# Performance work log

Measured on AMD Instinct MI355X. Metric: run time of the kernel, lower is better.

The kernel has to match this reference:

```python
import jax, jax.numpy as jnp
import numpy as np

T = 16384
INPUT_SIZE = 1024
STATE_SIZE = 512

def _xavier(key, shape):
    fan_in, fan_out = shape[-1], shape[-2] if len(shape) > 1 else shape[-1]
    bound = float(np.sqrt(6.0 / (fan_in + fan_out)))
    return jax.random.uniform(key, shape, jnp.float32, -bound, bound)

def setup_inputs() -> dict:
    key = jax.random.key(0)
    ks = jax.random.split(key, 6)
    x = jax.random.normal(ks[0], (T, INPUT_SIZE), jnp.float32)
    weight_input = _xavier(ks[1], (STATE_SIZE, 4, INPUT_SIZE))
    weight_recur = _xavier(ks[2], (4, STATE_SIZE))
    bias = _xavier(ks[3], (4, STATE_SIZE))
    W_reg = _xavier(ks[4], (1, STATE_SIZE))
    b_reg = jnp.zeros((1,), jnp.float32)
    return {"x": x, "weight_input": weight_input, "weight_recur": weight_recur,
            "bias": bias, "W_reg": W_reg, "b_reg": b_reg}

def reference(x, weight_input, weight_recur, bias, W_reg, b_reg):
    S = weight_recur.shape[1]
    # Precompute per-step input contributions: u[t, g, s] = weight_input[s, g, :] . x[t]
    u = jnp.einsum('sgi,ti->tgs', weight_input, x)  # (T, 4, S)

    def step(carry, u_t):
        h, c = carry  # each (S,)
        # torch: addmm(bias, weight_recur, diag(h)) == bias + weight_recur * h
        gates = bias + weight_recur * h[None, :] + u_t  # (4, S)
        f, i, o, g = gates
        f = jax.nn.sigmoid(f)
        i = jax.nn.sigmoid(i)
        o = jax.nn.sigmoid(o)
        g = jnp.tanh(g)
        c1 = f * c + i * g           # torch: f @ diag(c) + i*g
        h1 = o * jnp.tanh(c1)        # torch: diag of o * tanh(diag(c1))
        return (h1, c1), (h1, c1)

    h0 = jnp.zeros((S,), x.dtype)
    c0 = jnp.zeros((S,), x.dtype)
    (_, _), (hs, cs) = jax.lax.scan(step, (h0, c0), u)
    h_n = jnp.concatenate([h0[None, :], hs], axis=0)  # (T+1, S)
    c_n = jnp.concatenate([c0[None, :], cs], axis=0)  # (T+1, S)
    q = h_n @ W_reg.T + b_reg  # (T+1, 1); dropout p=0 -> identity
    q_t = q[1:]                # (T, 1)
    return (q_t, h_n, c_n)
```

## Files before the change

### kernel.cpp

```cpp
#include <hip/hip_runtime.h>

typedef unsigned short u16;
typedef unsigned int u32;
typedef __attribute__((ext_vector_type(4))) unsigned short u16x4;
typedef __attribute__((ext_vector_type(8))) short short8;
typedef __attribute__((ext_vector_type(8))) __bf16 bf16x8;
typedef __attribute__((ext_vector_type(4))) float f32x4;

#define T_STEPS 16384
#define INP 1024
#define SDIM 512
#define NGEMM 2048
#define L2E 1.4426950408889634f

__device__ __forceinline__ u16 f2bf(float f) {
    unsigned u = __float_as_uint(f);
    return (u16)((u + 0x7fffu + ((u >> 16) & 1u)) >> 16);
}
__device__ __forceinline__ float bfhi(u32 d) { return __uint_as_float(d & 0xffff0000u); }
__device__ __forceinline__ float bflo(u32 d) { return __uint_as_float(d << 16); }

__device__ __forceinline__ void gload_lds16(const void* g, void* l) {
    __builtin_amdgcn_global_load_lds((const __attribute__((address_space(1))) unsigned*)g,
                                     (__attribute__((address_space(3))) unsigned*)l, 16, 0, 0);
}

__global__ void cvt_x(const float* __restrict__ x, u16* __restrict__ xb, long n4) {
    long i = (long)blockIdx.x * blockDim.x + threadIdx.x;
    long stride = (long)gridDim.x * blockDim.x;
    for (; i < n4; i += stride) {
        float4 v = ((const float4*)x)[i];
        u16x4 o;
        o.x = f2bf(v.x); o.y = f2bf(v.y); o.z = f2bf(v.z); o.w = f2bf(v.w);
        ((u16x4*)xb)[i] = o;
    }
}

__global__ void pack_w(const float* __restrict__ w, u16* __restrict__ wb) {
    int id = blockIdx.x * blockDim.x + threadIdx.x;
    int kv = id & 255;
    int n  = id >> 8;
    int g = n >> 9, s = n & 511;
    const float4 v = *(const float4*)(w + ((long)(s * 4 + g)) * INP + kv * 4);
    u16x4 o;
    o.x = f2bf(v.x); o.y = f2bf(v.y); o.z = f2bf(v.z); o.w = f2bf(v.w);
    *(u16x4*)(wb + (long)n * INP + kv * 4) = o;
}

__global__ __launch_bounds__(512, 2) void gemm_bt(const u16* __restrict__ A,
                                                  const u16* __restrict__ B,
                                                  const float* __restrict__ wrec,
                                                  const float* __restrict__ bsv,
                                                  u32* __restrict__ coef,
                                                  int M, int N, int K) {
    __shared__ u16 sA[5][256 * 32];
    __shared__ u16 sB[5][256 * 32];
    const int tid = threadIdx.x;
    const int nbx = N >> 8;
    const int nwg = gridDim.x;
    const int cpx = nwg >> 3;
    const int bid = ((int)blockIdx.x & 7) * cpx + ((int)blockIdx.x >> 3);
    const int bx = bid % nbx, by = bid / nbx;
    const long brow = (long)by << 8, bcol = (long)bx << 8;
    const int w = tid >> 6, lane = tid & 63;
    const int wr = w >> 2, wc = w & 3;
    const int r16 = lane & 15, kq = lane >> 4;

    const int row0  = w * 32 + (lane >> 2);
    const int sslot = lane & 3;
    const int chs   = sslot ^ ((row0 >> 1) & 3);
    const u16* gA0 = A + (brow + row0) * (long)K + chs * 8;
    const u16* gA1 = gA0 + 16 * (long)K;
    const u16* gB0 = B + (bcol + row0) * (long)K + chs * 8;
    const u16* gB1 = gB0 + 16 * (long)K;
    const int dst0 = row0 * 32 + sslot * 8;
    const int dst1 = dst0 + 16 * 32;

    const int slotR = kq ^ ((r16 >> 1) & 3);
    int aoff[8], boff[4];
    #pragma unroll
    for (int m = 0; m < 8; ++m)
        aoff[m] = (wr * 128 + m * 16 + r16) * 32 + slotR * 8;
    #pragma unroll
    for (int n = 0; n < 4; ++n)
        boff[n] = (wc * 64 + n * 16 + r16) * 32 + slotR * 8;

    f32x4 acc[8][4] = {};
    bf16x8 afr[8], bfr[4];

#define STAGE(BUF, koff) do { \
        gload_lds16(gA0 + (koff), &sA[BUF][dst0]); \
        gload_lds16(gA1 + (koff), &sA[BUF][dst1]); \
        gload_lds16(gB0 + (koff), &sB[BUF][dst0]); \
        gload_lds16(gB1 + (koff), &sB[BUF][dst1]); \
    } while (0)

#define ITER(BNXT, SBUF, SKOFF, WAITSTR, DOSTAGE, DOREAD) do { \
        __builtin_amdgcn_s_setprio(1); \
        _Pragma("unroll") for (int m_ = 0; m_ < 8; ++m_) { \
            _Pragma("unroll") for (int n_ = 0; n_ < 4; ++n_) \
                acc[m_][n_] = __builtin_amdgcn_mfma_f32_16x16x32_bf16(afr[m_], bfr[n_], acc[m_][n_], 0, 0, 0); \
            if (DOREAD) afr[m_] = *(const bf16x8*)&sA[BNXT][aoff[m_]]; \
        } \
        __builtin_amdgcn_s_setprio(0); \
        if (DOREAD) { \
            _Pragma("unroll") for (int n_ = 0; n_ < 4; ++n_) \
                bfr[n_] = *(const bf16x8*)&sB[BNXT][boff[n_]]; \
        } \
        asm volatile(WAITSTR ::: "memory"); \
        if (DOSTAGE) { STAGE(SBUF, SKOFF); } \
        __builtin_amdgcn_s_barrier(); \
    } while (0)

    STAGE(0, 0);
    STAGE(1, 32);
    STAGE(2, 64);
    STAGE(3, 96);
    asm volatile("s_waitcnt vmcnt(8)" ::: "memory");
    __builtin_amdgcn_s_barrier();
    afr[0] = *(const bf16x8*)&sA[0][aoff[0]];
    #pragma unroll
    for (int n_ = 0; n_ < 4; ++n_) bfr[n_] = *(const bf16x8*)&sB[0][boff[n_]];
    #pragma unroll
    for (int m_ = 1; m_ < 8; ++m_) afr[m_] = *(const bf16x8*)&sA[0][aoff[m_]];

    #pragma unroll 1
    for (int t = 0; t < 25; t += 5) {
        ITER(1, 4, (t + 4) * 32, "s_waitcnt vmcnt(4)", 1, 1);
        ITER(2, 0, (t + 5) * 32, "s_waitcnt vmcnt(4)", 1, 1);
        ITER(3, 1, (t + 6) * 32, "s_waitcnt vmcnt(4)", 1, 1);
        ITER(4, 2, (t + 7) * 32, "s_waitcnt vmcnt(4)", 1, 1);
        ITER(0, 3, (t + 8) * 32, "s_waitcnt vmcnt(4)", 1, 1);
    }
    ITER(1, 4, 29 * 32, "s_waitcnt vmcnt(4)", 1, 1);
    ITER(2, 0, 30 * 32, "s_waitcnt vmcnt(4)", 1, 1);
    ITER(3, 1, 31 * 32, "s_waitcnt vmcnt(4)", 1, 1);
    ITER(4, 0, 0,       "s_waitcnt vmcnt(4)", 0, 1);
    ITER(0, 0, 0,       "s_waitcnt vmcnt(0)", 0, 1);
    ITER(1, 0, 0,       "s_waitcnt vmcnt(0)", 0, 1);
    {
        __builtin_amdgcn_s_setprio(1);
        #pragma unroll
        for (int m_ = 0; m_ < 8; ++m_)
            #pragma unroll
            for (int n_ = 0; n_ < 4; ++n_)
                acc[m_][n_] = __builtin_amdgcn_mfma_f32_16x16x32_bf16(afr[m_], bfr[n_], acc[m_][n_], 0, 0, 0);
        __builtin_amdgcn_s_setprio(0);
    }
#undef ITER
#undef STAGE

    const int g = (int)(bcol >> 9);
    float wvv[4], bvv[4];
    #pragma unroll
    for (int n = 0; n < 4; ++n) {
        long col = bcol + wc * 64 + n * 16 + r16;
        wvv[n] = wrec[col]; bvv[n] = bsv[col];
    }
    #pragma unroll
    for (int m = 0; m < 8; ++m) {
        #pragma unroll
        for (int j = 0; j < 4; ++j) {
            u32 pk[4];
            #pragma unroll
            for (int n = 0; n < 4; ++n) {
                float z0 = acc[m][n][j] + bvv[n];
                if (g == 3) {
                    float et = __builtin_amdgcn_exp2f(-2.f * L2E * z0);
                    float r = __builtin_amdgcn_rcpf(1.f + et);
                    float t = __builtin_fmaf(2.f, r, -1.f);
                    pk[n] = ((u32)f2bf(t) << 16) | f2bf((1.f - t * t) * wvv[n]);
                } else {
                    float e = __builtin_amdgcn_exp2f(-L2E * z0);
                    float r = __builtin_amdgcn_rcpf(1.f + e);
                    float kk = (g == 0) ? 1.f : ((g == 1) ? (-2.f * L2E) : 2.f);
                    float C0 = kk * r;
                    pk[n] = ((u32)f2bf(C0) << 16) | f2bf(C0 * r * e * wvv[n]);
                }
            }
            long row = brow + wr * 128 + m * 16 + kq * 4 + j;
            uint4 v4; v4.x = pk[0]; v4.y = pk[1]; v4.z = pk[2]; v4.w = pk[3];
            *(uint4*)(coef + row * NGEMM + bcol + wc * 64 + r16 * 4) = v4;
        }
    }
}

#define CHUNK 16
#define LCHUNK 128
#define NPAR (T_STEPS / LCHUNK)
#define WARMCH 4
#define PF 4

#define STEP(U) do { \
    float fh  = __builtin_fmaf(bflo((U)[0]), h, bfhi((U)[0])); \
    float ia  = __builtin_fmaf(bflo((U)[1]), h, bfhi((U)[1])); \
    float oo2 = __builtin_fmaf(bflo((U)[2]), h, bfhi((U)[2])); \
    float gb  = __builtin_fmaf(bflo((U)[3]), h, bfhi((U)[3])); \
    float ign = ia * gb; \
    float negoo = -0.5f * oo2; \
    c2 = __builtin_fmaf(fh, c2, ign); \
    float rt = __builtin_amdgcn_rcpf(1.f + __builtin_amdgcn_exp2f(c2)); \
    h = __builtin_fmaf(oo2, rt, negoo); \
    cval = c2 * CK; \
} while (0)

__global__ __launch_bounds__(128) void lstm_scan(const u32* __restrict__ coef,
                                                 float* __restrict__ h_out,
                                                 float* __restrict__ c_out) {
    __shared__ u32 lds[2][CHUNK][256];
    const int tid = threadIdx.x;
    const int lane = tid & 63;
    const int blk_ch = blockIdx.x & 7;
    const int chunk = blockIdx.x >> 3;
    const int warm = (chunk == 0) ? 0 : WARMCH;
    const long tstart = (long)chunk * LCHUNK - (long)warm * CHUNK;
    const int NC = LCHUNK / CHUNK + warm;

    if (tid >= 64) {
        const u32* src = coef + tstart * NGEMM + (lane >> 4) * SDIM + blk_ch * 64 + (lane & 15) * 4;
        #pragma unroll 8
        for (int j = 0; j < CHUNK; ++j)
            gload_lds16(src + (long)j * NGEMM, &lds[0][j][0]);
        __syncthreads();
        for (int k = 0; k < NC; ++k) {
            if (k + 1 < NC) {
                const u32* s2 = src + (long)(k + 1) * CHUNK * NGEMM;
                u32* dst = &lds[(k + 1) & 1][0][0];
                #pragma unroll 8
                for (int j = 0; j < CHUNK; ++j)
                    gload_lds16(s2 + (long)j * NGEMM, dst + j * 256);
            }
            __syncthreads();
        }
        return;
    }

    const int s = blk_ch * 64 + (lane & 3) * 16 + (lane >> 2);
    const float CK = -0.34657359027997264f;
    if (chunk == 0) { h_out[s] = 0.f; c_out[s] = 0.f; }
    float h = 0.f, c2 = 0.f, cval = 0.f;
    float* hp = h_out + SDIM + s;
    float* cp = c_out + SDIM + s;

    __syncthreads();
    for (int k = 0; k < NC; ++k) {
        const u32* Ld = &lds[k & 1][0][0];
        u32 R[PF][4];
        #pragma unroll
        for (int p = 0; p < PF; ++p) {
            R[p][0] = Ld[p * 256 + lane];
            R[p][1] = Ld[p * 256 + 64 + lane];
            R[p][2] = Ld[p * 256 + 128 + lane];
            R[p][3] = Ld[p * 256 + 192 + lane];
        }
        const long tbase = tstart + (long)k * CHUNK;
        if (k < warm) {
            #pragma unroll
            for (int j = 0; j < CHUNK; ++j) {
                STEP(R[j & (PF - 1)]);
                if (j < CHUNK - PF) {
                    R[j & (PF - 1)][0] = Ld[(j + PF) * 256 + lane];
                    R[j & (PF - 1)][1] = Ld[(j + PF) * 256 + 64 + lane];
                    R[j & (PF - 1)][2] = Ld[(j + PF) * 256 + 128 + lane];
                    R[j & (PF - 1)][3] = Ld[(j + PF) * 256 + 192 + lane];
                }
            }
        } else {
            #pragma unroll
            for (int j = 0; j < CHUNK; ++j) {
                STEP(R[j & (PF - 1)]);
                hp[(tbase + j) * SDIM] = h;
                cp[(tbase + j) * SDIM] = cval;
                if (j < CHUNK - PF) {
                    R[j & (PF - 1)][0] = Ld[(j + PF) * 256 + lane];
                    R[j & (PF - 1)][1] = Ld[(j + PF) * 256 + 64 + lane];
                    R[j & (PF - 1)][2] = Ld[(j + PF) * 256 + 128 + lane];
                    R[j & (PF - 1)][3] = Ld[(j + PF) * 256 + 192 + lane];
                }
            }
        }
        __syncthreads();
    }
}

__global__ __launch_bounds__(256) void q_kernel(const float* __restrict__ h_n,
                                                const float* __restrict__ wreg,
                                                const float* __restrict__ breg,
                                                float* __restrict__ q) {
    int gw = (blockIdx.x * blockDim.x + threadIdx.x) >> 6;
    int lane = threadIdx.x & 63;
    if (gw >= T_STEPS) return;
    const float* row = h_n + (long)(gw + 1) * SDIM;
    float sum = 0.f;
    #pragma unroll
    for (int j = 0; j < 8; ++j)
        sum += row[lane + j * 64] * wreg[lane + j * 64];
    #pragma unroll
    for (int off = 32; off > 0; off >>= 1)
        sum += __shfl_down(sum, off, 64);
    if (lane == 0) q[gw] = sum + breg[0];
}

extern "C" void kernel_launch(void* const* d_in, const int* in_sizes, int n_in,
                              void* d_out, int out_size, void* d_ws, size_t ws_size,
                              hipStream_t stream) {
    const float* x     = (const float*)d_in[0];
    const float* w_in  = (const float*)d_in[1];
    const float* w_rec = (const float*)d_in[2];
    const float* bias  = (const float*)d_in[3];
    const float* w_reg = (const float*)d_in[4];
    const float* b_reg = (const float*)d_in[5];

    float* out = (float*)d_out;
    float* q   = out;
    float* h_n = out + T_STEPS;
    float* c_n = h_n + (long)(T_STEPS + 1) * SDIM;

    char* ws = (char*)d_ws;
    const size_t COEF_BYTES = (size_t)T_STEPS * NGEMM * 4;
    const size_t XB_BYTES   = (size_t)T_STEPS * INP * 2;
    u32* coef = (u32*)ws;
    u16* xb   = (u16*)(ws + COEF_BYTES);
    u16* wb   = (u16*)(ws + COEF_BYTES + XB_BYTES);

    cvt_x<<<4096, 256, 0, stream>>>(x, xb, (long)T_STEPS * INP / 4);
    pack_w<<<2048, 256, 0, stream>>>(w_in, wb);
    gemm_bt<<<(T_STEPS / 256) * (NGEMM / 256), 512, 0, stream>>>(xb, wb, w_rec, bias, coef, T_STEPS, NGEMM, INP);
    lstm_scan<<<8 * NPAR, 128, 0, stream>>>(coef, h_n, c_n);
    q_kernel<<<(T_STEPS * 64) / 256, 256, 0, stream>>>(h_n, w_reg, b_reg, q);
}
```

Baseline: 146.3 us.

## Fuse q projection into LSTM scan with per-slice partial sums

Computes each timestep's partial dot product of h with W_reg inside the scan, using a wave shuffle reduction over the 64 state elements a block owns. The partials go to a small workspace buffer, and a light q_reduce kernel sums the 8 slices and adds the bias. This avoids re-reading the whole h_n array in a separate kernel. The cost is a 6-step shuffle reduction on the serial critical path of every scan step, which may slow the latency-bound recurrence. The qpart buffer reuses the xb workspace region, which is dead by the time the scan runs.

New measurement: 154.4 us. 1.06x slower.

```diff
diff --git a/kernel.cpp b/kernel.cpp
--- a/kernel.cpp
+++ b/kernel.cpp
@@ -205,8 +205,10 @@
 } while (0)
 
 __global__ __launch_bounds__(128) void lstm_scan(const u32* __restrict__ coef,
+                                                 const float* __restrict__ wqreg,
                                                  float* __restrict__ h_out,
-                                                 float* __restrict__ c_out) {
+                                                 float* __restrict__ c_out,
+                                                 float* __restrict__ qpart) {
     __shared__ u32 lds[2][CHUNK][256];
     const int tid = threadIdx.x;
     const int lane = tid & 63;
@@ -237,10 +239,12 @@
 
     const int s = blk_ch * 64 + (lane & 3) * 16 + (lane >> 2);
     const float CK = -0.34657359027997264f;
+    const float wq = wqreg[s];
     if (chunk == 0) { h_out[s] = 0.f; c_out[s] = 0.f; }
     float h = 0.f, c2 = 0.f, cval = 0.f;
     float* hp = h_out + SDIM + s;
     float* cp = c_out + SDIM + s;
+    float* qp = qpart + (long)blk_ch * T_STEPS;
 
     __syncthreads();
     for (int k = 0; k < NC; ++k) {
@@ -271,6 +275,11 @@
                 STEP(R[j & (PF - 1)]);
                 hp[(tbase + j) * SDIM] = h;
                 cp[(tbase + j) * SDIM] = cval;
+                float p = h * wq;
+                #pragma unroll
+                for (int off = 32; off > 0; off >>= 1)
+                    p += __shfl_down(p, off, 64);
+                if (lane == 0) qp[tbase + j] = p;
                 if (j < CHUNK - PF) {
                     R[j & (PF - 1)][0] = Ld[(j + PF) * 256 + lane];
                     R[j & (PF - 1)][1] = Ld[(j + PF) * 256 + 64 + lane];
@@ -283,22 +292,15 @@
     }
 }
 
-__global__ __launch_bounds__(256) void q_kernel(const float* __restrict__ h_n,
-                                                const float* __restrict__ wreg,
+__global__ __launch_bounds__(256) void q_reduce(const float* __restrict__ qpart,
                                                 const float* __restrict__ breg,
                                                 float* __restrict__ q) {
-    int gw = (blockIdx.x * blockDim.x + threadIdx.x) >> 6;
-    int lane = threadIdx.x & 63;
-    if (gw >= T_STEPS) return;
-    const float* row = h_n + (long)(gw + 1) * SDIM;
-    float sum = 0.f;
-    #pragma unroll
-    for (int j = 0; j < 8; ++j)
-        sum += row[lane + j * 64] * wreg[lane + j * 64];
-    #pragma unroll
-    for (int off = 32; off > 0; off >>= 1)
-        sum += __shfl_down(sum, off, 64);
-    if (lane == 0) q[gw] = sum + breg[0];
+    int t = blockIdx.x * 256 + threadIdx.x;
+    float sum = breg[0];
+    #pragma unroll
+    for (int g = 0; g < 8; ++g)
+        sum += qpart[(long)g * T_STEPS + t];
+    q[t] = sum;
 }
 
 extern "C" void kernel_launch(void* const* d_in, const int* in_sizes, int n_in,
@@ -322,10 +324,11 @@
     u32* coef = (u32*)ws;
     u16* xb   = (u16*)(ws + COEF_BYTES);
     u16* wb   = (u16*)(ws + COEF_BYTES + XB_BYTES);
+    float* qpart = (float*)(ws + COEF_BYTES);
 
     cvt_x<<<4096, 256, 0, stream>>>(x, xb, (long)T_STEPS * INP / 4);
     pack_w<<<2048, 256, 0, stream>>>(w_in, wb);
     gemm_bt<<<(T_STEPS / 256) * (NGEMM / 256), 512, 0, stream>>>(xb, wb, w_rec, bias, coef, T_STEPS, NGEMM, INP);
-    lstm_scan<<<8 * NPAR, 128, 0, stream>>>(coef, h_n, c_n);
-    q_kernel<<<(T_STEPS * 64) / 256, 256, 0, stream>>>(h_n, w_reg, b_reg, q);
-}
+    lstm_scan<<<8 * NPAR, 128, 0, stream>>>(coef, w_reg, h_n, c_n, qpart);
+    q_reduce<<<T_STEPS / 256, 256, 0, stream>>>(qpart, b_reg, q);
+}
```
